# Performance work log

Measured on AMD Instinct MI355X. Metric: run time of the kernel, lower is better.

The kernel has to match this reference:

```python
import jax, jax.numpy as jnp
import numpy as np

EPS = 1e-7
DIM_PRIMARY = 8  # param.dim_primary_caps, used for attention_coef


def squash(v):
    # Squash (Mazzia et al. 2021): coef = 1 - exp(-||v||); unit = v / (||v|| + eps)
    norm = jnp.linalg.norm(v, axis=-1, keepdims=True)
    coef = 1.0 - 1.0 / jnp.exp(norm)
    return coef * v / (norm + EPS)


def setup_inputs() -> dict:
    key = jax.random.key(0)
    k1, k2, k3 = jax.random.split(key, 3)
    B, N, Dp = 16, 1152, 8   # batch, num_primary_caps, dim_primary_caps
    M, Dd = 10, 16           # num_digit_caps, dim_digit_caps
    primary_caps = jax.random.normal(k1, (B, N, Dp), dtype=jnp.float32)
    W = jax.random.normal(k2, (M, N, Dd, Dp), dtype=jnp.float32) * 0.05
    B_prior = jax.random.normal(k3, (M, 1, N), dtype=jnp.float32) * 0.05
    return {"primary_caps": primary_caps, "W": W, "B_prior": B_prior}


def reference(primary_caps, W, B_prior):
    coef = 1.0 / jnp.sqrt(jnp.float32(DIM_PRIMARY))
    # U_hat[b,m,n,d] = W[m,n,d,p] @ u[b,n,p]  (fused batched GEMM, replaces tf.map_fn)
    U_hat = jnp.einsum('mndp,bnp->bmnd', W, primary_caps)
    # attention scores A[b,m,n,k]
    A = coef * jnp.einsum('bmnd,bmkd->bmnk', U_hat, U_hat)
    # reduce over axis -2 (keepdims) then softmax over axis -2 (size-1 axis),
    # exactly as in the original code
    C = jax.nn.softmax(jnp.sum(A, axis=-2, keepdims=True), axis=-2)  # [b,m,1,n]
    CB = (C + B_prior[None])[:, :, 0, :]                             # [b,m,n]
    S = jnp.einsum('bmn,bmnd->bmd', CB, U_hat)                       # [b,m,d]
    return squash(S)
```

## Files before the change

kernel.cpp:

```cpp
#include <hip/hip_runtime.h>
#include <math.h>

#define BSZ   16
#define NCAPS 1152
#define DP    8
#define MCAPS 10
#define DD    16

#define NC     24
#define NCHUNK (NCAPS / NC)

__global__ __launch_bounds__(256) void digitcaps_partial(
    const float* __restrict__ u,
    const float* __restrict__ W,
    const float* __restrict__ Bp,
    float* __restrict__ part)
{
    __shared__ float w_t[NC][DD][DP];
    __shared__ float u_t[BSZ][NC][DP];
    __shared__ float bp_t[NC];

    const int t  = threadIdx.x;
    const int m  = blockIdx.x / NCHUNK;
    const int n0 = (blockIdx.x % NCHUNK) * NC;

    const float4* wg = (const float4*)(W + ((size_t)(m * NCAPS + n0)) * DD * DP);
    float4* wl = (float4*)&w_t[0][0][0];
#pragma unroll
    for (int i = 0; i < 3; ++i) {
        wl[t + 256 * i] = wg[t + 256 * i];
    }

    float4* ul = (float4*)&u_t[0][0][0];
#pragma unroll
    for (int i = 0; i < 3; ++i) {
        int idx = t + 256 * i;
        int b   = idx / (NC * DP / 4);
        int off = idx % (NC * DP / 4);
        ul[idx] = ((const float4*)(u + ((size_t)(b * NCAPS + n0)) * DP))[off];
    }

    if (t < NC) bp_t[t] = 1.0f + Bp[m * NCAPS + n0 + t];
    __syncthreads();

    const int b = t >> 4;
    const int d = t & 15;

    float acc = 0.0f;
#pragma unroll
    for (int n = 0; n < NC; ++n) {
        const float4 w0 = *(const float4*)&w_t[n][d][0];
        const float4 w1 = *(const float4*)&w_t[n][d][4];
        const float4 u0 = *(const float4*)&u_t[b][n][0];
        const float4 u1 = *(const float4*)&u_t[b][n][4];
        float dot = w0.x * u0.x + w0.y * u0.y + w0.z * u0.z + w0.w * u0.w
                  + w1.x * u1.x + w1.y * u1.y + w1.z * u1.z + w1.w * u1.w;
        acc += bp_t[n] * dot;
    }

    part[(size_t)blockIdx.x * 256 + t] = acc;
}

__global__ __launch_bounds__(256) void digitcaps_reduce_squash(
    const float* __restrict__ part,
    float* __restrict__ out)
{
    const int g  = blockIdx.x * 256 + threadIdx.x;
    const int d  = g & 15;
    const int bm = g >> 4;
    const int m  = bm % MCAPS;
    const int b  = bm / MCAPS;

    float s = 0.0f;
#pragma unroll
    for (int c = 0; c < NCHUNK; ++c) {
        s += part[(((size_t)(m * NCHUNK + c) * BSZ + b) << 4) + d];
    }

    float ss = s * s;
#pragma unroll
    for (int w = 1; w < 16; w <<= 1) {
        ss += __shfl_xor(ss, w, 16);
    }

    float norm  = sqrtf(ss);
    float scale = (1.0f - expf(-norm)) / (norm + 1e-7f);
    out[g] = scale * s;
}

extern "C" void kernel_launch(void* const* d_in, const int* in_sizes, int n_in,
                              void* d_out, int out_size, void* d_ws, size_t ws_size,
                              hipStream_t stream) {
    const float* u  = (const float*)d_in[0];
    const float* W  = (const float*)d_in[1];
    const float* Bp = (const float*)d_in[2];
    float* out  = (float*)d_out;
    float* part = (float*)d_ws;

    digitcaps_partial<<<dim3(MCAPS * NCHUNK), dim3(256), 0, stream>>>(u, W, Bp, part);
    digitcaps_reduce_squash<<<dim3(MCAPS), dim3(256), 0, stream>>>(part, out);
}
```

Baseline: 66.73 us.

## Fuse partial sums and squash into one kernel per batch-capsule pair

Replaces the two-kernel chunked partial-sum plus reduce/squash pipeline with a single kernel where each block handles one (batch, digit capsule) pair over all primary capsules, reducing in shared memory and applying squash in place. The block index is swizzled so that blocks sharing the same W slice are spread to exploit cache sharing. This removes the second launch and the workspace round trip, but W is now read once per batch rather than once overall, relying on L2 reuse, and the grid shrinks to 160 blocks.

```diff
diff --git a/kernel.cpp b/kernel.cpp
--- a/kernel.cpp
+++ b/kernel.cpp
@@ -7,85 +7,71 @@
 #define MCAPS 10
 #define DD    16
 
-#define NC     24
-#define NCHUNK (NCAPS / NC)
-
-__global__ __launch_bounds__(256) void digitcaps_partial(
+__global__ __launch_bounds__(256) void digitcaps_fused(
     const float* __restrict__ u,
     const float* __restrict__ W,
     const float* __restrict__ Bp,
-    float* __restrict__ part)
+    float* __restrict__ out)
 {
-    __shared__ float w_t[NC][DD][DP];
-    __shared__ float u_t[BSZ][NC][DP];
-    __shared__ float bp_t[NC];
+    __shared__ float u_t[NCAPS][DP];
+    __shared__ float bp_t[NCAPS];
+    __shared__ float red[16][DD];
 
-    const int t  = threadIdx.x;
-    const int m  = blockIdx.x / NCHUNK;
-    const int n0 = (blockIdx.x % NCHUNK) * NC;
+    const int t = threadIdx.x;
 
-    const float4* wg = (const float4*)(W + ((size_t)(m * NCAPS + n0)) * DD * DP);
-    float4* wl = (float4*)&w_t[0][0][0];
+    const int p = (blockIdx.x & 7) * 20 + (blockIdx.x >> 3);
+    const int m = p >> 4;
+    const int b = p & 15;
+
+    {
+        const float4* ug = (const float4*)(u + (size_t)b * NCAPS * DP);
+        float4* ul = (float4*)&u_t[0][0];
 #pragma unroll
-    for (int i = 0; i < 3; ++i) {
-        wl[t + 256 * i] = wg[t + 256 * i];
+        for (int i = 0; i < 9; ++i) ul[t + 256 * i] = ug[t + 256 * i];
+
+        const float4* bg = (const float4*)(Bp + (size_t)m * NCAPS);
+        float4* bl = (float4*)bp_t;
+        bl[t] = bg[t];
+        if (t < 32) bl[256 + t] = bg[256 + t];
+    }
+    __syncthreads();
+
+    const int d  = t & 15;
+    const int ng = t >> 4;
+
+    const float* wp = W + (size_t)m * NCAPS * DD * DP
+                        + (size_t)ng * DD * DP
+                        + (size_t)d * DP;
+
+    float acc = 0.0f;
+#pragma unroll 8
+    for (int i = 0; i < NCAPS / 16; ++i) {
+        const int n = i * 16 + ng;
+        const float4 w0 = *(const float4*)(wp + (size_t)i * 16 * DD * DP);
+        const float4 w1 = *(const float4*)(wp + (size_t)i * 16 * DD * DP + 4);
+        const float4 u0 = *(const float4*)&u_t[n][0];
+        const float4 u1 = *(const float4*)&u_t[n][4];
+        float dot = w0.x * u0.x + w0.y * u0.y + w0.z * u0.z + w0.w * u0.w
+                  + w1.x * u1.x + w1.y * u1.y + w1.z * u1.z + w1.w * u1.w;
+        acc = fmaf(1.0f + bp_t[n], dot, acc);
     }
 
-    float4* ul = (float4*)&u_t[0][0][0];
-#pragma unroll
-    for (int i = 0; i < 3; ++i) {
-        int idx = t + 256 * i;
-        int b   = idx / (NC * DP / 4);
-        int off = idx % (NC * DP / 4);
-        ul[idx] = ((const float4*)(u + ((size_t)(b * NCAPS + n0)) * DP))[off];
-    }
-
-    if (t < NC) bp_t[t] = 1.0f + Bp[m * NCAPS + n0 + t];
+    red[ng][d] = acc;
     __syncthreads();
 
-    const int b = t >> 4;
-    const int d = t & 15;
+    if (t < DD) {
+        float s = 0.0f;
+#pragma unroll
+        for (int g = 0; g < 16; ++g) s += red[g][t];
 
-    float acc = 0.0f;
+        float ss = s * s;
 #pragma unroll
-    for (int n = 0; n < NC; ++n) {
-        const float4 w0 = *(const float4*)&w_t[n][d][0];
-        const float4 w1 = *(const float4*)&w_t[n][d][4];
-        const float4 u0 = *(const float4*)&u_t[b][n][0];
-        const float4 u1 = *(const float4*)&u_t[b][n][4];
-        float dot = w0.x * u0.x + w0.y * u0.y + w0.z * u0.z + w0.w * u0.w
-                  + w1.x * u1.x + w1.y * u1.y + w1.z * u1.z + w1.w * u1.w;
-        acc += bp_t[n] * dot;
+        for (int w = 1; w < 16; w <<= 1) ss += __shfl_xor(ss, w, 16);
+
+        float norm  = sqrtf(ss);
+        float scale = (1.0f - expf(-norm)) / (norm + 1e-7f);
+        out[(b * MCAPS + m) * DD + t] = scale * s;
     }
-
-    part[(size_t)blockIdx.x * 256 + t] = acc;
-}
-
-__global__ __launch_bounds__(256) void digitcaps_reduce_squash(
-    const float* __restrict__ part,
-    float* __restrict__ out)
-{
-    const int g  = blockIdx.x * 256 + threadIdx.x;
-    const int d  = g & 15;
-    const int bm = g >> 4;
-    const int m  = bm % MCAPS;
-    const int b  = bm / MCAPS;
-
-    float s = 0.0f;
-#pragma unroll
-    for (int c = 0; c < NCHUNK; ++c) {
-        s += part[(((size_t)(m * NCHUNK + c) * BSZ + b) << 4) + d];
-    }
-
-    float ss = s * s;
-#pragma unroll
-    for (int w = 1; w < 16; w <<= 1) {
-        ss += __shfl_xor(ss, w, 16);
-    }
-
-    float norm  = sqrtf(ss);
-    float scale = (1.0f - expf(-norm)) / (norm + 1e-7f);
-    out[g] = scale * s;
 }
 
 extern "C" void kernel_launch(void* const* d_in, const int* in_sizes, int n_in,
@@ -94,9 +80,8 @@
     const float* u  = (const float*)d_in[0];
     const float* W  = (const float*)d_in[1];
     const float* Bp = (const float*)d_in[2];
-    float* out  = (float*)d_out;
-    float* part = (float*)d_ws;
+    float* out = (float*)d_out;
+    (void)d_ws; (void)ws_size;
 
-    digitcaps_partial<<<dim3(MCAPS * NCHUNK), dim3(256), 0, stream>>>(u, W, Bp, part);
-    digitcaps_reduce_squash<<<dim3(MCAPS), dim3(256), 0, stream>>>(part, out);
+    digitcaps_fused<<<dim3(BSZ * MCAPS), dim3(256), 0, stream>>>(u, W, Bp, out);
 }
```

Result: slower. 68.53 us (+2.7%).

## Keep W in registers per thread, reduce over n with shuffles, widen final reduction

Applied to the files above, without the earlier changes.

Each thread now owns one (n, d) weight row held in registers, scaled by (1+B_prior), and computes all 16 batch dot products from shared u. Partial sums over the 16 capsules in a block are reduced with wave shuffles and a small shared array. The partial layout is transposed so the second kernel can launch 160 blocks of 64 threads doing coalesced reductions. The aim is to remove the W staging through LDS and to parallelise the final reduction, which previously ran on only 10 blocks with a serial loop. The cost is more blocks in the first kernel (chunk size 24 down to 16) and an extra sync plus shuffle reduction per block.

```diff
diff --git a/kernel.cpp b/kernel.cpp
--- a/kernel.cpp
+++ b/kernel.cpp
@@ -7,8 +7,8 @@
 #define MCAPS 10
 #define DD    16
 
-#define NC     24
-#define NCHUNK (NCAPS / NC)
+#define NC    16
+#define NCH   (NCAPS / NC)
 
 __global__ __launch_bounds__(256) void digitcaps_partial(
     const float* __restrict__ u,
@@ -16,76 +16,92 @@
     const float* __restrict__ Bp,
     float* __restrict__ part)
 {
-    __shared__ float w_t[NC][DD][DP];
     __shared__ float u_t[BSZ][NC][DP];
-    __shared__ float bp_t[NC];
+    __shared__ float red[4][BSZ][DD];
 
     const int t  = threadIdx.x;
-    const int m  = blockIdx.x / NCHUNK;
-    const int n0 = (blockIdx.x % NCHUNK) * NC;
+    const int m  = blockIdx.x / NCH;
+    const int c  = blockIdx.x % NCH;
+    const int n0 = c * NC;
 
-    const float4* wg = (const float4*)(W + ((size_t)(m * NCAPS + n0)) * DD * DP);
-    float4* wl = (float4*)&w_t[0][0][0];
+    const int d  = t & 15;
+    const int ng = t >> 4;
+
+    const float* wp = W + (((size_t)(m * NCAPS + n0 + ng)) * DD + d) * DP;
+    float4 w0 = *(const float4*)(wp);
+    float4 w1 = *(const float4*)(wp + 4);
+
+    {
+        float4* ul = (float4*)&u_t[0][0][0];
 #pragma unroll
-    for (int i = 0; i < 3; ++i) {
-        wl[t + 256 * i] = wg[t + 256 * i];
+        for (int i = 0; i < 2; ++i) {
+            int idx = t + 256 * i;
+            int b   = idx >> 5;
+            int off = idx & 31;
+            ul[idx] = ((const float4*)(u + ((size_t)b * NCAPS + n0) * DP))[off];
+        }
     }
 
-    float4* ul = (float4*)&u_t[0][0][0];
+    const float bpv = 1.0f + Bp[m * NCAPS + n0 + ng];
+    w0.x *= bpv; w0.y *= bpv; w0.z *= bpv; w0.w *= bpv;
+    w1.x *= bpv; w1.y *= bpv; w1.z *= bpv; w1.w *= bpv;
+
+    __syncthreads();
+
+    float acc[BSZ];
 #pragma unroll
-    for (int i = 0; i < 3; ++i) {
-        int idx = t + 256 * i;
-        int b   = idx / (NC * DP / 4);
-        int off = idx % (NC * DP / 4);
-        ul[idx] = ((const float4*)(u + ((size_t)(b * NCAPS + n0)) * DP))[off];
+    for (int b = 0; b < BSZ; ++b) {
+        const float4 u0 = *(const float4*)&u_t[b][ng][0];
+        const float4 u1 = *(const float4*)&u_t[b][ng][4];
+        acc[b] = w0.x * u0.x + w0.y * u0.y + w0.z * u0.z + w0.w * u0.w
+               + w1.x * u1.x + w1.y * u1.y + w1.z * u1.z + w1.w * u1.w;
     }
 
-    if (t < NC) bp_t[t] = 1.0f + Bp[m * NCAPS + n0 + t];
+    const int wv   = t >> 6;
+    const int lane = t & 63;
+#pragma unroll
+    for (int b = 0; b < BSZ; ++b) {
+        float v = acc[b];
+        v += __shfl_xor(v, 16);
+        v += __shfl_xor(v, 32);
+        if (lane < 16) red[wv][b][lane] = v;
+    }
     __syncthreads();
 
-    const int b = t >> 4;
-    const int d = t & 15;
+    const int b2 = t >> 4;
+    float s = red[0][b2][d] + red[1][b2][d] + red[2][b2][d] + red[3][b2][d];
 
-    float acc = 0.0f;
-#pragma unroll
-    for (int n = 0; n < NC; ++n) {
-        const float4 w0 = *(const float4*)&w_t[n][d][0];
-        const float4 w1 = *(const float4*)&w_t[n][d][4];
-        const float4 u0 = *(const float4*)&u_t[b][n][0];
-        const float4 u1 = *(const float4*)&u_t[b][n][4];
-        float dot = w0.x * u0.x + w0.y * u0.y + w0.z * u0.z + w0.w * u0.w
-                  + w1.x * u1.x + w1.y * u1.y + w1.z * u1.z + w1.w * u1.w;
-        acc += bp_t[n] * dot;
-    }
-
-    part[(size_t)blockIdx.x * 256 + t] = acc;
+    part[(((size_t)(m * BSZ + b2)) * NCH + c) * DD + d] = s;
 }
 
-__global__ __launch_bounds__(256) void digitcaps_reduce_squash(
+__global__ __launch_bounds__(64) void digitcaps_reduce_squash(
     const float* __restrict__ part,
     float* __restrict__ out)
 {
-    const int g  = blockIdx.x * 256 + threadIdx.x;
-    const int d  = g & 15;
-    const int bm = g >> 4;
+    const int bm = blockIdx.x;
     const int m  = bm % MCAPS;
-    const int b  = bm / MCAPS;
+    const int bb = bm / MCAPS;
+
+    const int l = threadIdx.x;
+    const float* p = part + ((size_t)(m * BSZ + bb)) * NCH * DD;
 
     float s = 0.0f;
 #pragma unroll
-    for (int c = 0; c < NCHUNK; ++c) {
-        s += part[(((size_t)(m * NCHUNK + c) * BSZ + b) << 4) + d];
+    for (int i = 0; i < (NCH * DD) / 64; ++i) {
+        s += p[i * 64 + l];
     }
+    s += __shfl_xor(s, 16);
+    s += __shfl_xor(s, 32);
 
     float ss = s * s;
 #pragma unroll
-    for (int w = 1; w < 16; w <<= 1) {
-        ss += __shfl_xor(ss, w, 16);
+    for (int w = 1; w < 16; w <<= 1) ss += __shfl_xor(ss, w, 16);
+
+    if (l < DD) {
+        float norm  = sqrtf(ss);
+        float scale = (1.0f - expf(-norm)) / (norm + 1e-7f);
+        out[(bb * MCAPS + m) * DD + l] = scale * s;
     }
-
-    float norm  = sqrtf(ss);
-    float scale = (1.0f - expf(-norm)) / (norm + 1e-7f);
-    out[g] = scale * s;
 }
 
 extern "C" void kernel_launch(void* const* d_in, const int* in_sizes, int n_in,
@@ -97,6 +113,6 @@
     float* out  = (float*)d_out;
     float* part = (float*)d_ws;
 
-    digitcaps_partial<<<dim3(MCAPS * NCHUNK), dim3(256), 0, stream>>>(u, W, Bp, part);
-    digitcaps_reduce_squash<<<dim3(MCAPS), dim3(256), 0, stream>>>(part, out);
+    digitcaps_partial<<<dim3(MCAPS * NCH), dim3(256), 0, stream>>>(u, W, Bp, part);
+    digitcaps_reduce_squash<<<dim3(BSZ * MCAPS), dim3(64), 0, stream>>>(part, out);
 }
```

After: 63.99 us. 4.1% less time.
